# Performance work log

Hardware: AMD Instinct MI355X
Metric: run time of the kernel (lower is better)

The kernel has to match this reference:

```python
import jax, jax.numpy as jnp
import numpy as np

WINDOW = 100   # window_size
HEADS = 8      # num_heads
KDIM = 64      # Keras MHA key_dim (= value_dim by default)
D = 512        # model dim (query/key/value feature dim)
B = 8
L = 4096       # not a multiple of WINDOW -> pad_len = 4


def setup_inputs() -> dict:
    key = jax.random.key(0)
    ks = jax.random.split(key, 5)
    s = 0.02  # small init scale like glorot
    return {
        "x":  jax.random.normal(ks[0], (B, L, D), jnp.float32),
        "Wq": jax.random.normal(ks[1], (D, HEADS, KDIM), jnp.float32) * s,
        "bq": jnp.zeros((HEADS, KDIM), jnp.float32),
        "Wk": jax.random.normal(ks[2], (D, HEADS, KDIM), jnp.float32) * s,
        "bk": jnp.zeros((HEADS, KDIM), jnp.float32),
        "Wv": jax.random.normal(ks[3], (D, HEADS, KDIM), jnp.float32) * s,
        "bv": jnp.zeros((HEADS, KDIM), jnp.float32),
        "Wo": jax.random.normal(ks[4], (HEADS, KDIM, D), jnp.float32) * s,
        "bo": jnp.zeros((D,), jnp.float32),
    }


def reference(x, Wq, bq, Wk, bk, Wv, bv, Wo, bo):
    Bx, Lx, Dx = x.shape
    pad_len = (WINDOW - Lx % WINDOW) % WINDOW
    xp = jnp.pad(x, ((0, 0), (0, pad_len), (0, 0)))          # [B, L+pad, D]
    n_win = (Lx + pad_len) // WINDOW
    xw = xp.reshape(Bx * n_win, WINDOW, Dx)                  # [B*N, W, D]

    # Keras MultiHeadAttention(num_heads=HEADS, key_dim=KDIM), self-attention
    q = jnp.einsum('bwd,dhk->bwhk', xw, Wq) + bq             # [B*N, W, H, K]
    k = jnp.einsum('bwd,dhk->bwhk', xw, Wk) + bk
    v = jnp.einsum('bwd,dhk->bwhk', xw, Wv) + bv

    scale = 1.0 / np.sqrt(KDIM).astype(np.float32)
    scores = jnp.einsum('bqhk,bshk->bhqs', q, k) * scale     # [B*N, H, W, W]
    attn = jax.nn.softmax(scores, axis=-1)
    o = jnp.einsum('bhqs,bshk->bqhk', attn, v)               # [B*N, W, H, K]
    y = jnp.einsum('bqhk,hkd->bqd', o, Wo) + bo              # [B*N, W, D]

    return y.reshape(Bx, n_win, WINDOW, Dx)                  # pad_len is static (=4 here)
```

## Files before the change

kernel.cpp:

```cpp
#include <hip/hip_runtime.h>

typedef unsigned short u16;
typedef __attribute__((ext_vector_type(4))) float f32x4;
typedef __attribute__((ext_vector_type(8))) short short8;

#define WIN_SZ 100
#define NWIN 41
#define NBATCH 8
#define SEQ 4096
#define DM 512
#define NHEAD 8
#define KD 64
#define NWINS (NBATCH * NWIN)
#define MROWS (NWINS * WIN_SZ)
#define MBLKS 257
#define TOKPB (NWIN * WIN_SZ)
#define NQKV 1536

#define OFF_XBF   0u
#define OFF_OBUF  16793600u
#define OFF_WQKVT 33587200u
#define OFF_WOT   34373632u
#define OFF_ZBLK  34635776u
#define OFF_BIAS  34636032u
#define OFF_BIAS2 34639104u

__device__ __forceinline__ u16 f2bf(float f) {
  union { float f; unsigned i; } v; v.f = f;
  unsigned r = (v.i + 0x7fffu + ((v.i >> 16) & 1u)) >> 16;
  return (u16)r;
}

__device__ __forceinline__ void gl2lds16(const void* g, void* lds) {
  __builtin_amdgcn_global_load_lds(
      (const __attribute__((address_space(1))) void*)g,
      (__attribute__((address_space(3))) void*)lds, 16, 0, 0);
}

__global__ void prep_k(const float* __restrict__ Wq, const float* __restrict__ Wk,
                       const float* __restrict__ Wv, const float* __restrict__ Wo,
                       const float* __restrict__ bq, const float* __restrict__ bk,
                       const float* __restrict__ bv, const float* __restrict__ bo,
                       u16* __restrict__ ws) {
  __shared__ u16 tile[64][65];
  const int z = blockIdx.z;
  const float* src = (z == 0) ? Wq : (z == 1) ? Wk : (z == 2) ? Wv : Wo;
  u16* dst = (z < 3) ? (ws + OFF_WQKVT + (unsigned)z * 512u * 512u)
                     : (ws + OFF_WOT);
  const int k0 = blockIdx.y * 64, n0 = blockIdx.x * 64;
  const int t = threadIdx.x;
  const int c = t & 63, r4 = t >> 6;
#pragma unroll
  for (int p = 0; p < 16; ++p) {
    int r = p * 4 + r4;
    tile[r][c] = f2bf(src[(size_t)(k0 + r) * 512 + n0 + c]);
  }
  __syncthreads();
#pragma unroll
  for (int p = 0; p < 16; ++p) {
    int r = p * 4 + r4;
    dst[(size_t)(n0 + r) * 512 + k0 + c] = tile[c][r];
  }
  if (blockIdx.x == 0 && blockIdx.y == 0) {
    float* biasF = (float*)(ws + OFF_BIAS);
    float* biasO = (float*)(ws + OFF_BIAS2);
    for (int j = t; j < 512; j += 256) {
      if (z == 0) biasF[j] = bq[j];
      else if (z == 1) biasF[512 + j] = bk[j];
      else if (z == 2) biasF[1024 + j] = bv[j];
      else biasO[j] = bo[j];
    }
    if (z == 3 && t < 128) ws[OFF_ZBLK + t] = 0;
  }
}

__global__ void convx_k(const float* __restrict__ x, u16* __restrict__ ws) {
  u16* xbf = ws + OFF_XBF;
  int i = blockIdx.x * 256 + threadIdx.x;
  if (i >= MROWS * 128) return;
  int m = i >> 7;
  int c4 = (i & 127) * 4;
  int b = m / TOKPB, tk = m - b * TOKPB;
  float4 v = make_float4(0.f, 0.f, 0.f, 0.f);
  if (tk < SEQ) v = *(const float4*)(x + (size_t)(b * SEQ + tk) * DM + c4);
  u16 o[4] = {f2bf(v.x), f2bf(v.y), f2bf(v.z), f2bf(v.w)};
  *(uint2*)(xbf + (size_t)m * DM + c4) = *(const uint2*)o;
}

#define QKS 72
#define PS 136
#define SM_ELEMS 24832

__global__ __launch_bounds__(256, 3)
void qkvattn_k(const u16* __restrict__ ws) {
  __shared__ u16 smem[SM_ELEMS];
  u16* Xs  = smem;
  u16* Wsl = smem + 7168;
  u16* Vt  = smem;
  u16* Qs  = smem + 8704;
  u16* Ks  = smem + 16768;
  u16* P   = smem + 8704;

  const int win = blockIdx.x, h = blockIdx.y;
  const int t = threadIdx.x, w = t >> 6, l = t & 63;
  const int q = l >> 4, cl = l & 15;
  const int lc = (t & 7) * 8;

  unsigned xoff[4];
#pragma unroll
  for (int i = 0; i < 4; ++i) {
    int m = i * 32 + (t >> 3);
    xoff[i] = (m < WIN_SZ)
                  ? (OFF_XBF + (unsigned)(win * WIN_SZ + m) * DM + lc)
                  : OFF_ZBLK;
  }
  unsigned woff[6];
#pragma unroll
  for (int i = 0; i < 6; ++i) {
    int g = i * 32 + (t >> 3);
    unsigned nrow = (unsigned)(g >> 6) * 512u + (unsigned)h * 64u + (g & 63);
    woff[i] = OFF_WQKVT + nrow * DM + lc;
  }

  f32x4 acc_p[7][3] = {};
  for (int k0 = 0; k0 < DM; k0 += 64) {
    __syncthreads();
#pragma unroll
    for (int i = 0; i < 4; ++i)
      if (i * 32 + w * 8 < 112)
        gl2lds16(ws + xoff[i] + (xoff[i] == OFF_ZBLK ? 0u : (unsigned)k0),
                 &Xs[(i * 32 + w * 8) * 64]);
#pragma unroll
    for (int i = 0; i < 6; ++i)
      gl2lds16(ws + woff[i] + k0, &Wsl[(i * 32 + w * 8) * 64]);
    __syncthreads();
#pragma unroll
    for (int ks = 0; ks < 2; ++ks) {
      const int ko = ks * 32 + q * 8;
      short8 af[7], bf[3];
#pragma unroll
      for (int mt = 0; mt < 7; ++mt)
        af[mt] = *(const short8*)&Xs[(mt * 16 + cl) * 64 + ko];
#pragma unroll
      for (int ntl = 0; ntl < 3; ++ntl)
        bf[ntl] = *(const short8*)&Wsl[((3 * w + ntl) * 16 + cl) * 64 + ko];
#pragma unroll
      for (int mt = 0; mt < 7; ++mt)
#pragma unroll
        for (int ntl = 0; ntl < 3; ++ntl)
          acc_p[mt][ntl] = __builtin_amdgcn_mfma_f32_16x16x32_bf16(
              af[mt], bf[ntl], acc_p[mt][ntl], 0, 0, 0);
    }
  }
  __syncthreads();

  {
    const float* biasF = (const float*)(ws + OFF_BIAS);
#pragma unroll
    for (int ntl = 0; ntl < 3; ++ntl) {
      const int nt = 3 * w + ntl;
      const int cw = (nt & 3) * 16 + cl;
      const float bb = biasF[(nt >> 2) * 512 + h * 64 + cw];
#pragma unroll
      for (int mt = 0; mt < 7; ++mt)
#pragma unroll
        for (int r = 0; r < 4; ++r) {
          const int tok = mt * 16 + q * 4 + r;
          const u16 v16 = f2bf(acc_p[mt][ntl][r] + bb);
          if (nt < 4) Qs[tok * QKS + cw] = v16;
          else if (nt < 8) Ks[tok * QKS + cw] = v16;
          else Vt[cw * PS + tok] = v16;
        }
    }
    for (int idx = t; idx < 64 * 24; idx += 256)
      Vt[(idx / 24) * PS + 112 + idx % 24] = 0;
  }
  __syncthreads();

  const int nmt = (w < 3) ? 2 : 1;
  const int mt0 = w, mt1 = w + 4;

  f32x4 accs[2][7];
#pragma unroll
  for (int im = 0; im < 2; ++im) {
    if (im < nmt) {
      const int mt = (im == 0) ? mt0 : mt1;
      const int ar = (mt * 16 + cl) * QKS + q * 8;
      short8 a0 = *(const short8*)&Qs[ar];
      short8 a1 = *(const short8*)&Qs[ar + 32];
#pragma unroll
      for (int nt = 0; nt < 7; ++nt) {
        const int br = (nt * 16 + cl) * QKS + q * 8;
        short8 b0 = *(const short8*)&Ks[br];
        short8 b1 = *(const short8*)&Ks[br + 32];
        f32x4 c = {};
        c = __builtin_amdgcn_mfma_f32_16x16x32_bf16(a0, b0, c, 0, 0, 0);
        c = __builtin_amdgcn_mfma_f32_16x16x32_bf16(a1, b1, c, 0, 0, 0);
        accs[im][nt] = c;
      }
    }
  }

  const float scale = 0.125f;
#pragma unroll
  for (int im = 0; im < 2; ++im) {
    if (im < nmt) {
#pragma unroll
      for (int r = 0; r < 4; ++r) {
        float mx = -1e30f;
#pragma unroll
        for (int nt = 0; nt < 7; ++nt) {
          float s = accs[im][nt][r] * scale;
          if ((nt < 6) || (cl < 4)) mx = fmaxf(mx, s);
        }
        mx = fmaxf(mx, __shfl_xor(mx, 1, 64));
        mx = fmaxf(mx, __shfl_xor(mx, 2, 64));
        mx = fmaxf(mx, __shfl_xor(mx, 4, 64));
        mx = fmaxf(mx, __shfl_xor(mx, 8, 64));
        float sum = 0.f;
#pragma unroll
        for (int nt = 0; nt < 7; ++nt) {
          float s = accs[im][nt][r] * scale;
          bool valid = (nt < 6) || (cl < 4);
          float e = valid ? __expf(s - mx) : 0.f;
          accs[im][nt][r] = e;
          sum += e;
        }
        sum += __shfl_xor(sum, 1, 64);
        sum += __shfl_xor(sum, 2, 64);
        sum += __shfl_xor(sum, 4, 64);
        sum += __shfl_xor(sum, 8, 64);
        float inv = 1.0f / sum;
#pragma unroll
        for (int nt = 0; nt < 7; ++nt) accs[im][nt][r] *= inv;
      }
    }
  }
  __syncthreads();

#pragma unroll
  for (int im = 0; im < 2; ++im) {
    if (im < nmt) {
      const int mt = (im == 0) ? mt0 : mt1;
#pragma unroll
      for (int nt = 0; nt < 7; ++nt)
#pragma unroll
        for (int r = 0; r < 4; ++r)
          P[(mt * 16 + q * 4 + r) * PS + nt * 16 + cl] = f2bf(accs[im][nt][r]);
    }
  }
  for (int idx = t; idx < 112 * 24; idx += 256)
    P[(idx / 24) * PS + 112 + idx % 24] = 0;
  __syncthreads();

  f32x4 acco[2][4] = {};
#pragma unroll
  for (int ks = 0; ks < 4; ++ks) {
    const int ko = ks * 32 + q * 8;
    short8 a0 = *(const short8*)&P[(mt0 * 16 + cl) * PS + ko];
    short8 a1 = a0;
    if (nmt == 2) a1 = *(const short8*)&P[(mt1 * 16 + cl) * PS + ko];
#pragma unroll
    for (int nt = 0; nt < 4; ++nt) {
      short8 b = *(const short8*)&Vt[(nt * 16 + cl) * PS + ko];
      acco[0][nt] = __builtin_amdgcn_mfma_f32_16x16x32_bf16(a0, b, acco[0][nt], 0, 0, 0);
      if (nmt == 2)
        acco[1][nt] = __builtin_amdgcn_mfma_f32_16x16x32_bf16(a1, b, acco[1][nt], 0, 0, 0);
    }
  }

  u16* obuf = (u16*)(ws + OFF_OBUF);
  const size_t orow0 = (size_t)win * WIN_SZ;
#pragma unroll
  for (int im = 0; im < 2; ++im) {
    if (im < nmt) {
      const int mt = (im == 0) ? mt0 : mt1;
#pragma unroll
      for (int nt = 0; nt < 4; ++nt)
#pragma unroll
        for (int r = 0; r < 4; ++r) {
          int row = mt * 16 + q * 4 + r;
          if (row < WIN_SZ)
            obuf[(orow0 + row) * DM + h * KD + nt * 16 + cl] = f2bf(acco[im][nt][r]);
        }
    }
  }
}

__global__ __launch_bounds__(256, 4)
void gemm_k(const u16* __restrict__ ws, unsigned aoff0, unsigned btoff,
            unsigned biasoff, float* __restrict__ Cout, int Ntot) {
  __shared__ u16 Alds[128 * 64];
  __shared__ u16 Blds[128 * 64];

  const int t = threadIdx.x;
  const int w = t >> 6;
  const int l = t & 63;
  const int nb = blockIdx.x, mb = blockIdx.y;
  const int m0 = mb * 128, n0 = nb * 128;
  const int lr = t >> 3;
  const int lc = (t & 7) * 8;

  unsigned aoff[4], boff[4];
#pragma unroll
  for (int i = 0; i < 4; ++i) {
    int m = m0 + i * 32 + lr;
    aoff[i] = (m < MROWS) ? (aoff0 + (unsigned)m * DM + lc) : OFF_ZBLK;
    boff[i] = btoff + (unsigned)(n0 + i * 32 + lr) * DM + lc;
  }

  f32x4 acc[4][4] = {};
  const int wm = (w & 1) * 64;
  const int wn = (w >> 1) * 64;
  const int q = l >> 4, cl = l & 15;

  for (int k0 = 0; k0 < DM; k0 += 64) {
    __syncthreads();
#pragma unroll
    for (int i = 0; i < 4; ++i) {
      gl2lds16(ws + aoff[i] + (aoff[i] == OFF_ZBLK ? 0u : (unsigned)k0),
               &Alds[(i * 32 + w * 8) * 64]);
      gl2lds16(ws + boff[i] + k0, &Blds[(i * 32 + w * 8) * 64]);
    }
    __syncthreads();
#pragma unroll
    for (int ks = 0; ks < 2; ++ks) {
      short8 av[4], bv_[4];
      const int ko = ks * 32 + q * 8;
#pragma unroll
      for (int mi = 0; mi < 4; ++mi)
        av[mi] = *(const short8*)&Alds[(wm + mi * 16 + cl) * 64 + ko];
#pragma unroll
      for (int ni = 0; ni < 4; ++ni)
        bv_[ni] = *(const short8*)&Blds[(wn + ni * 16 + cl) * 64 + ko];
#pragma unroll
      for (int mi = 0; mi < 4; ++mi)
#pragma unroll
        for (int ni = 0; ni < 4; ++ni)
          acc[mi][ni] = __builtin_amdgcn_mfma_f32_16x16x32_bf16(
              av[mi], bv_[ni], acc[mi][ni], 0, 0, 0);
    }
  }

  const float* biasF = (const float*)(ws + biasoff);
#pragma unroll
  for (int mi = 0; mi < 4; ++mi) {
#pragma unroll
    for (int ni = 0; ni < 4; ++ni) {
      int col = n0 + wn + ni * 16 + cl;
      float bb = biasF[col];
#pragma unroll
      for (int r = 0; r < 4; ++r) {
        int row = m0 + wm + mi * 16 + q * 4 + r;
        if (row < MROWS)
          Cout[(size_t)row * Ntot + col] = acc[mi][ni][r] + bb;
      }
    }
  }
}

extern "C" void kernel_launch(void* const* d_in, const int* in_sizes, int n_in,
                              void* d_out, int out_size, void* d_ws, size_t ws_size,
                              hipStream_t stream) {
  const float* x  = (const float*)d_in[0];
  const float* Wq = (const float*)d_in[1];
  const float* bq = (const float*)d_in[2];
  const float* Wk = (const float*)d_in[3];
  const float* bk = (const float*)d_in[4];
  const float* Wv = (const float*)d_in[5];
  const float* bv = (const float*)d_in[6];
  const float* Wo = (const float*)d_in[7];
  const float* bo = (const float*)d_in[8];

  u16* ws = (u16*)d_ws;

  prep_k<<<dim3(8, 8, 4), dim3(256), 0, stream>>>(
      Wq, Wk, Wv, Wo, bq, bk, bv, bo, ws);
  convx_k<<<dim3((MROWS * 128 + 255) / 256), dim3(256), 0, stream>>>(x, ws);
  qkvattn_k<<<dim3(NWINS, NHEAD), dim3(256), 0, stream>>>(ws);
  gemm_k<<<dim3(DM / 128, MBLKS), dim3(256), 0, stream>>>(
      ws, OFF_OBUF, OFF_WOT, OFF_BIAS2, (float*)d_out, DM);
}
```

Measured before the change: 284.0 us.

## Double-buffer LDS staging with 32-wide K slices in QKV-attention and GEMM kernels

Both the fused QKV+attention kernel and the output-projection GEMM now stage K in 32-element slices into two alternating LDS buffers. The next slice's global-to-LDS copy is issued before the MFMAs on the current slice, so each iteration needs one barrier instead of two. This is meant to hide global load latency behind MFMA work. The trade-off is twice as many loop iterations, a different per-wave load mapping using masks for padded rows, and LDS reads at a 32-element row stride that may cause more bank conflicts.

Result: slower. 329.0 us (+15.9%).

```diff
diff --git a/kernel.cpp b/kernel.cpp
--- a/kernel.cpp
+++ b/kernel.cpp
@@ -90,12 +90,11 @@
 #define QKS 72
 #define PS 136
 #define SM_ELEMS 24832
+#define STG_BUF 9728
 
 __global__ __launch_bounds__(256, 3)
 void qkvattn_k(const u16* __restrict__ ws) {
   __shared__ u16 smem[SM_ELEMS];
-  u16* Xs  = smem;
-  u16* Wsl = smem + 7168;
   u16* Vt  = smem;
   u16* Qs  = smem + 8704;
   u16* Ks  = smem + 16768;
@@ -104,55 +103,65 @@
   const int win = blockIdx.x, h = blockIdx.y;
   const int t = threadIdx.x, w = t >> 6, l = t & 63;
   const int q = l >> 4, cl = l & 15;
-  const int lc = (t & 7) * 8;
-
-  unsigned xoff[4];
-#pragma unroll
-  for (int i = 0; i < 4; ++i) {
-    int m = i * 32 + (t >> 3);
-    xoff[i] = (m < WIN_SZ)
-                  ? (OFF_XBF + (unsigned)(win * WIN_SZ + m) * DM + lc)
-                  : OFF_ZBLK;
-  }
-  unsigned woff[6];
-#pragma unroll
-  for (int i = 0; i < 6; ++i) {
-    int g = i * 32 + (t >> 3);
-    unsigned nrow = (unsigned)(g >> 6) * 512u + (unsigned)h * 64u + (g & 63);
-    woff[i] = OFF_WQKVT + nrow * DM + lc;
+
+  unsigned ssrc[5], smask[5], sdst[5];
+  int cnt = 0;
+#pragma unroll
+  for (int j = 0; j < 5; ++j) {
+    const int id = w + j * 4;
+    if (id < 19) {
+      if (id < 7) {
+        const int m = id * 16 + (l >> 2);
+        const bool real = (m < WIN_SZ);
+        ssrc[cnt] = real ? (OFF_XBF + (unsigned)(win * WIN_SZ + m) * DM + (unsigned)(l & 3) * 8u)
+                         : OFF_ZBLK;
+        smask[cnt] = real ? 0xFFFFFFFFu : 0u;
+        sdst[cnt] = (unsigned)id * 512u;
+      } else {
+        const int g = (id - 7) * 16 + (l >> 2);
+        const unsigned nrow = (unsigned)(g >> 6) * 512u + (unsigned)h * 64u + (unsigned)(g & 63);
+        ssrc[cnt] = OFF_WQKVT + nrow * DM + (unsigned)(l & 3) * 8u;
+        smask[cnt] = 0xFFFFFFFFu;
+        sdst[cnt] = 3584u + (unsigned)(id - 7) * 512u;
+      }
+      ++cnt;
+    }
   }
 
   f32x4 acc_p[7][3] = {};
-  for (int k0 = 0; k0 < DM; k0 += 64) {
+
+#pragma unroll
+  for (int j = 0; j < 5; ++j)
+    if (j < cnt) gl2lds16(ws + ssrc[j], &smem[sdst[j]]);
+  __syncthreads();
+
+  for (int it = 0; it < 16; ++it) {
+    const int cur = it & 1;
+    if (it < 15) {
+      const unsigned k0n = (unsigned)(it + 1) * 32u;
+      const unsigned bb = (unsigned)(cur ^ 1) * STG_BUF;
+#pragma unroll
+      for (int j = 0; j < 5; ++j)
+        if (j < cnt) gl2lds16(ws + ssrc[j] + (k0n & smask[j]), &smem[bb + sdst[j]]);
+    }
+    const u16* Xb = smem + cur * STG_BUF;
+    const u16* Wb = Xb + 3584;
+    const int ko = q * 8;
+    short8 af[7], bf[3];
+#pragma unroll
+    for (int mt = 0; mt < 7; ++mt)
+      af[mt] = *(const short8*)&Xb[(mt * 16 + cl) * 32 + ko];
+#pragma unroll
+    for (int ntl = 0; ntl < 3; ++ntl)
+      bf[ntl] = *(const short8*)&Wb[((3 * w + ntl) * 16 + cl) * 32 + ko];
+#pragma unroll
+    for (int mt = 0; mt < 7; ++mt)
+#pragma unroll
+      for (int ntl = 0; ntl < 3; ++ntl)
+        acc_p[mt][ntl] = __builtin_amdgcn_mfma_f32_16x16x32_bf16(
+            af[mt], bf[ntl], acc_p[mt][ntl], 0, 0, 0);
     __syncthreads();
-#pragma unroll
-    for (int i = 0; i < 4; ++i)
-      if (i * 32 + w * 8 < 112)
-        gl2lds16(ws + xoff[i] + (xoff[i] == OFF_ZBLK ? 0u : (unsigned)k0),
-                 &Xs[(i * 32 + w * 8) * 64]);
-#pragma unroll
-    for (int i = 0; i < 6; ++i)
-      gl2lds16(ws + woff[i] + k0, &Wsl[(i * 32 + w * 8) * 64]);
-    __syncthreads();
-#pragma unroll
-    for (int ks = 0; ks < 2; ++ks) {
-      const int ko = ks * 32 + q * 8;
-      short8 af[7], bf[3];
-#pragma unroll
-      for (int mt = 0; mt < 7; ++mt)
-        af[mt] = *(const short8*)&Xs[(mt * 16 + cl) * 64 + ko];
-#pragma unroll
-      for (int ntl = 0; ntl < 3; ++ntl)
-        bf[ntl] = *(const short8*)&Wsl[((3 * w + ntl) * 16 + cl) * 64 + ko];
-#pragma unroll
-      for (int mt = 0; mt < 7; ++mt)
-#pragma unroll
-        for (int ntl = 0; ntl < 3; ++ntl)
-          acc_p[mt][ntl] = __builtin_amdgcn_mfma_f32_16x16x32_bf16(
-              af[mt], bf[ntl], acc_p[mt][ntl], 0, 0, 0);
-    }
-  }
-  __syncthreads();
+  }
 
   {
     const float* biasF = (const float*)(ws + OFF_BIAS);
@@ -290,56 +299,66 @@
 __global__ __launch_bounds__(256, 4)
 void gemm_k(const u16* __restrict__ ws, unsigned aoff0, unsigned btoff,
             unsigned biasoff, float* __restrict__ Cout, int Ntot) {
-  __shared__ u16 Alds[128 * 64];
-  __shared__ u16 Blds[128 * 64];
+  __shared__ u16 smg[2][8192];
 
   const int t = threadIdx.x;
   const int w = t >> 6;
   const int l = t & 63;
   const int nb = blockIdx.x, mb = blockIdx.y;
   const int m0 = mb * 128, n0 = nb * 128;
-  const int lr = t >> 3;
-  const int lc = (t & 7) * 8;
-
-  unsigned aoff[4], boff[4];
-#pragma unroll
-  for (int i = 0; i < 4; ++i) {
-    int m = m0 + i * 32 + lr;
-    aoff[i] = (m < MROWS) ? (aoff0 + (unsigned)m * DM + lc) : OFF_ZBLK;
-    boff[i] = btoff + (unsigned)(n0 + i * 32 + lr) * DM + lc;
+  const int q = l >> 4, cl = l & 15;
+
+  unsigned ssrc[4], smask[4], sdst[4];
+#pragma unroll
+  for (int j = 0; j < 4; ++j) {
+    const int id = w + j * 4;
+    if (id < 8) {
+      const int m = m0 + id * 16 + (l >> 2);
+      const bool real = (m < MROWS);
+      ssrc[j] = real ? (aoff0 + (unsigned)m * DM + (unsigned)(l & 3) * 8u) : OFF_ZBLK;
+      smask[j] = real ? 0xFFFFFFFFu : 0u;
+      sdst[j] = (unsigned)id * 512u;
+    } else {
+      const int n = n0 + (id - 8) * 16 + (l >> 2);
+      ssrc[j] = btoff + (unsigned)n * DM + (unsigned)(l & 3) * 8u;
+      smask[j] = 0xFFFFFFFFu;
+      sdst[j] = 4096u + (unsigned)(id - 8) * 512u;
+    }
   }
 
   f32x4 acc[4][4] = {};
   const int wm = (w & 1) * 64;
   const int wn = (w >> 1) * 64;
-  const int q = l >> 4, cl = l & 15;
-
-  for (int k0 = 0; k0 < DM; k0 += 64) {
+
+#pragma unroll
+  for (int j = 0; j < 4; ++j) gl2lds16(ws + ssrc[j], &smg[0][sdst[j]]);
+  __syncthreads();
+
+  for (int it = 0; it < 16; ++it) {
+    const int cur = it & 1;
+    if (it < 15) {
+      const unsigned k0n = (unsigned)(it + 1) * 32u;
+#pragma unroll
+      for (int j = 0; j < 4; ++j)
+        gl2lds16(ws + ssrc[j] + (k0n & smask[j]), &smg[cur ^ 1][sdst[j]]);
+    }
+    const u16* Ab = smg[cur];
+    const u16* Bb = Ab + 4096;
+    const int ko = q * 8;
+    short8 av[4], bv_[4];
+#pragma unroll
+    for (int mi = 0; mi < 4; ++mi)
+      av[mi] = *(const short8*)&Ab[(wm + mi * 16 + cl) * 32 + ko];
+#pragma unroll
+    for (int ni = 0; ni < 4; ++ni)
+      bv_[ni] = *(const short8*)&Bb[(wn + ni * 16 + cl) * 32 + ko];
+#pragma unroll
+    for (int mi = 0; mi < 4; ++mi)
+#pragma unroll
+      for (int ni = 0; ni < 4; ++ni)
+        acc[mi][ni] = __builtin_amdgcn_mfma_f32_16x16x32_bf16(
+            av[mi], bv_[ni], acc[mi][ni], 0, 0, 0);
     __syncthreads();
-#pragma unroll
-    for (int i = 0; i < 4; ++i) {
-      gl2lds16(ws + aoff[i] + (aoff[i] == OFF_ZBLK ? 0u : (unsigned)k0),
-               &Alds[(i * 32 + w * 8) * 64]);
-      gl2lds16(ws + boff[i] + k0, &Blds[(i * 32 + w * 8) * 64]);
-    }
-    __syncthreads();
-#pragma unroll
-    for (int ks = 0; ks < 2; ++ks) {
-      short8 av[4], bv_[4];
-      const int ko = ks * 32 + q * 8;
-#pragma unroll
-      for (int mi = 0; mi < 4; ++mi)
-        av[mi] = *(const short8*)&Alds[(wm + mi * 16 + cl) * 64 + ko];
-#pragma unroll
-      for (int ni = 0; ni < 4; ++ni)
-        bv_[ni] = *(const short8*)&Blds[(wn + ni * 16 + cl) * 64 + ko];
-#pragma unroll
-      for (int mi = 0; mi < 4; ++mi)
-#pragma unroll
-        for (int ni = 0; ni < 4; ++ni)
-          acc[mi][ni] = __builtin_amdgcn_mfma_f32_16x16x32_bf16(
-              av[mi], bv_[ni], acc[mi][ni], 0, 0, 0);
-    }
   }
 
   const float* biasF = (const float*)(ws + biasoff);
```
